# Kernel tuning notes

Measured on AMD Instinct MI355X. Metric: run time of the kernel, lower is better.

## Reference

```python
import jax, jax.numpy as jnp
import numpy as np
import math

IN_CH, KEY_SIZE, VALUE_SIZE = 512, 64, 64
N, T = 4, 4096

def setup_inputs() -> dict:
    key = jax.random.key(0)
    ks = jax.random.split(key, 7)
    s_in = 1.0 / math.sqrt(IN_CH)
    return {
        "x": jax.random.normal(ks[0], (N, T, IN_CH), dtype=jnp.float32),
        "Wq": jax.random.uniform(ks[1], (IN_CH, KEY_SIZE), jnp.float32, -s_in, s_in),
        "bq": jax.random.uniform(ks[2], (KEY_SIZE,), jnp.float32, -s_in, s_in),
        "Wk": jax.random.uniform(ks[3], (IN_CH, KEY_SIZE), jnp.float32, -s_in, s_in),
        "bk": jax.random.uniform(ks[4], (KEY_SIZE,), jnp.float32, -s_in, s_in),
        "Wv": jax.random.uniform(ks[5], (IN_CH, VALUE_SIZE), jnp.float32, -s_in, s_in),
        "bv": jax.random.uniform(ks[6], (VALUE_SIZE,), jnp.float32, -s_in, s_in),
    }

def reference(x, Wq, bq, Wk, bk, Wv, bv):
    # x: [N, T, C]
    Tlen = x.shape[1]
    q = x @ Wq + bq              # [N, T, K]
    k = x @ Wk + bk              # [N, T, K]
    v = x @ Wv + bv              # [N, T, V]
    logits = jnp.einsum('ntk,nsk->nts', q, k)  # [N, T, T]
    # causal mask: strict upper triangle -> -inf (applied BEFORE scaling, as in the original)
    causal = jnp.tril(jnp.ones((Tlen, Tlen), dtype=bool))
    logits = jnp.where(causal, logits, -jnp.inf)
    scale = 1.0 / math.sqrt(Wq.shape[1])
    attn = jax.nn.softmax(logits * scale, axis=-1)
    read = jnp.einsum('nts,nsv->ntv', attn, v)  # [N, T, V]
    return jnp.concatenate((x, read), axis=2)   # [N, T, C+V]
```

## Files before the change

### kernel.cpp

```cpp
#include <hip/hip_runtime.h>
#include <stdint.h>

typedef __attribute__((ext_vector_type(8))) short bf16x8;
typedef __attribute__((ext_vector_type(4))) float f32x4;
typedef __attribute__((ext_vector_type(4))) unsigned short u16x4;
typedef unsigned short u16;

#define NBATCH 4
#define SEQ    4096
#define CIN    512
#define HD     64
#define OC     576
#define NROW   (NBATCH * SEQ)
#define KVB    262144

__device__ __forceinline__ float b2f(u16 u) {
    union { uint32_t i; float f; } w; w.i = ((uint32_t)u) << 16; return w.f;
}
__device__ __forceinline__ u16 f2b(float f) {
    union { float f; uint32_t i; } w; w.f = f;
    uint32_t r = w.i + 0x7fffu + ((w.i >> 16) & 1u);
    return (u16)(r >> 16);
}
__device__ __forceinline__ uint32_t cvtpk_bf16(float a, float b) {
    uint32_t r;
    asm("v_cvt_pk_bf16_f32 %0, %1, %2" : "=v"(r) : "v"(a), "v"(b));
    return r;
}

__global__ void prep_wt(const float* __restrict__ Wq, const float* __restrict__ Wk,
                        const float* __restrict__ Wv, u16* __restrict__ wt) {
    int row = blockIdx.x;
    int g = row >> 6, j = row & 63;
    const float* W = (g == 0) ? Wq : (g == 1) ? Wk : Wv;
    int nt = row >> 4, m = row & 15;
    for (int k = threadIdx.x; k < CIN; k += blockDim.x) {
        int c = k >> 5, qd = (k >> 3) & 3, jj = k & 7;
        size_t off = ((size_t)(nt * 16 + c) * 64 + qd * 16 + m) * 8 + jj;
        wt[off] = f2b(W[k * HD + j]);
    }
}

__global__ __launch_bounds__(256) void proj(
    const float* __restrict__ x, const u16* __restrict__ wt,
    const float* __restrict__ bq, const float* __restrict__ bk, const float* __restrict__ bv,
    u16* __restrict__ qb, u16* __restrict__ kbuf, u16* __restrict__ vtb,
    float* __restrict__ out)
{
    __shared__ __align__(16) float xs[32 * 512];

    int tid = threadIdx.x;
    int lane = tid & 63, w = tid >> 6;
    int m = lane & 15, quad = lane >> 4;
    int r0b = blockIdx.x * 32;

    {
        int rw = w >> 1;
        int pp = (w & 1) * 64 + lane;
#pragma unroll
        for (int k = 0; k < 16; k++) {
            int r = k * 2 + rw;
            int g = pp ^ (r & 15);
            const float* src = x + (size_t)(r0b + r) * CIN + g * 4;
            float* dst = xs + (size_t)(k * 256 + w * 64 + lane) * 4;
            __builtin_amdgcn_global_load_lds(
                (const __attribute__((address_space(1))) void*)src,
                (__attribute__((address_space(3))) void*)dst, 16, 0, 0);
        }
    }
    __syncthreads();

    int ntb = w * 3;

    f32x4 acc0[3], acc1[3];
#pragma unroll
    for (int i = 0; i < 3; i++) {
        acc0[i] = (f32x4){0.f, 0.f, 0.f, 0.f};
        acc1[i] = (f32x4){0.f, 0.f, 0.f, 0.f};
    }

    const float* xrow0 = xs + (size_t)m * 512;
    const float* xrow1 = xs + (size_t)(16 + m) * 512;

#pragma unroll
    for (int c = 0; c < 16; c++) {
        int L0 = c * 8 + quad * 2;
        f32x4 va0 = *(const f32x4*)(xrow0 + (size_t)((L0 ^ m) * 4));
        f32x4 vb0 = *(const f32x4*)(xrow0 + (size_t)(((L0 + 1) ^ m) * 4));
        f32x4 va1 = *(const f32x4*)(xrow1 + (size_t)((L0 ^ m) * 4));
        f32x4 vb1 = *(const f32x4*)(xrow1 + (size_t)(((L0 + 1) ^ m) * 4));
        bf16x8 a0, a1;
        {
            uint32_t* p0 = (uint32_t*)&a0;
            p0[0] = cvtpk_bf16(va0[0], va0[1]);
            p0[1] = cvtpk_bf16(va0[2], va0[3]);
            p0[2] = cvtpk_bf16(vb0[0], vb0[1]);
            p0[3] = cvtpk_bf16(vb0[2], vb0[3]);
            uint32_t* p1 = (uint32_t*)&a1;
            p1[0] = cvtpk_bf16(va1[0], va1[1]);
            p1[1] = cvtpk_bf16(va1[2], va1[3]);
            p1[2] = cvtpk_bf16(vb1[0], vb1[1]);
            p1[3] = cvtpk_bf16(vb1[2], vb1[3]);
        }
#pragma unroll
        for (int t = 0; t < 3; t++) {
            int nt = ntb + t;
            bf16x8 b = *(const bf16x8*)(wt + ((size_t)(nt * 16 + c) * 64 + quad * 16 + m) * 8);
            acc0[t] = __builtin_amdgcn_mfma_f32_16x16x32_bf16(a0, b, acc0[t], 0, 0, 0);
            acc1[t] = __builtin_amdgcn_mfma_f32_16x16x32_bf16(a1, b, acc1[t], 0, 0, 0);
        }
    }

#pragma unroll
    for (int k = 0; k < 16; k++) {
        int G = k * 256 + tid;
        int r = G >> 7, p = G & 127;
        f32x4 v = *(const f32x4*)(xs + (size_t)G * 4);
        int col = (p ^ (r & 15)) * 4;
        *(f32x4*)(out + (size_t)(r0b + r) * OC + col) = v;
    }

    const float SCQ = 0.125f * 1.44269504088896f;

#pragma unroll
    for (int tt = 0; tt < 2; tt++) {
        int r0 = r0b + tt * 16;
        int n  = r0 >> 12;
        int tl = r0 & (SEQ - 1);
#pragma unroll
        for (int t = 0; t < 3; t++) {
            f32x4 acc = tt ? acc1[t] : acc0[t];
            int nt = ntb + t;
            int bi = (nt & 3) * 16 + m;
            if (nt < 4) {
                float biasq = bq[bi];
#pragma unroll
                for (int reg = 0; reg < 4; reg++) {
                    size_t r = (size_t)(r0 + quad * 4 + reg);
                    qb[r * HD + bi] = f2b((acc[reg] + biasq) * SCQ);
                }
            } else if (nt < 8) {
                float biask = bk[bi];
                u16* kbase = kbuf + (size_t)n * KVB
                           + (((size_t)(tl >> 4) * 8 + (bi >> 3)) * 16) * 8 + (bi & 7);
#pragma unroll
                for (int reg = 0; reg < 4; reg++) {
                    int mkey = quad * 4 + reg;
                    kbase[(size_t)mkey * 8] = f2b(acc[reg] + biask);
                }
            } else {
                float biasv = bv[bi];
                u16x4 pk;
#pragma unroll
                for (int reg = 0; reg < 4; reg++) pk[reg] = f2b(acc[reg] + biasv);
                int key0 = tl + quad * 4;
                size_t off = ((((size_t)(bi >> 4) * 128 + (key0 >> 5)) * 4
                               + ((key0 >> 3) & 3)) * 16 + (bi & 15)) * 8 + (key0 & 7);
                *(u16x4*)(vtb + (size_t)n * KVB + off) = pk;
            }
        }
    }
}

__global__ __launch_bounds__(512, 2) void attn(
    const u16* __restrict__ qb, const u16* __restrict__ kbuf,
    const u16* __restrict__ vtb, float* __restrict__ out)
{
    __shared__ __align__(16) union {
        short p[8][16 * 72];
        float o[8][16][68];
    } lu;
    __shared__ float ldsm[8][16];
    __shared__ float ldsl[8][16];

    int tid = threadIdx.x;
    int lane = tid & 63, w = tid >> 6;
    int m = lane & 15, quad = lane >> 4;

    int idx = blockIdx.x;
    int xcd = idx & 7;
    int batch = xcd >> 1;
    int sub = (idx >> 3) * 2 + (xcd & 1);
    int jj = 127 - sub;
    int t0 = jj * 32;
    int nkb = (jj >> 1) + 1;
    int lastkb = nkb - 1;

    const u16* kpb = kbuf + (size_t)batch * KVB;
    const u16* vpb = vtb + (size_t)batch * KVB;

    bf16x8 ones;
#pragma unroll
    for (int i = 0; i < 8; i++) ones[i] = (short)0x3F80;

    const u16* qpb = qb + (size_t)(batch * SEQ + t0 + m) * HD + quad * 8;
    bf16x8 q0[2], q1[2];
#pragma unroll
    for (int q = 0; q < 2; q++) {
        q0[q] = *(const bf16x8*)(qpb + (size_t)(q * 16) * HD);
        q1[q] = *(const bf16x8*)(qpb + (size_t)(q * 16) * HD + 32);
    }

    float mst[2];
    f32x4 o[2][4], ol[2];
#pragma unroll
    for (int q = 0; q < 2; q++) {
        mst[q] = -1e30f;
        ol[q] = (f32x4){0.f, 0.f, 0.f, 0.f};
#pragma unroll
        for (int nt = 0; nt < 4; nt++) o[q][nt] = (f32x4){0.f, 0.f, 0.f, 0.f};
    }

    int cnt = (nkb > w) ? ((nkb - w + 7) >> 3) : 0;
    int kb = w;
    short* pw = &lu.p[w][0];

    bf16x8 k0[4], k1[4];
#pragma unroll
    for (int st = 0; st < 4; st++) {
        k0[st] = *(const bf16x8*)(kpb + (size_t)((kb * 4 + st) * 8 + quad) * 128 + m * 8);
        k1[st] = *(const bf16x8*)(kpb + (size_t)((kb * 4 + st) * 8 + quad + 4) * 128 + m * 8);
    }

    for (int it = 0; it < cnt; it++, kb += 8) {
        int s0 = kb * 64;
        bool diag = (kb == lastkb);

        bf16x8 vf0[4], vf1[4];
#pragma unroll
        for (int nt = 0; nt < 4; nt++) {
            vf0[nt] = *(const bf16x8*)(vpb + (size_t)((nt * 128 + (s0 >> 5)) * 4 + quad) * 128 + m * 8);
            vf1[nt] = *(const bf16x8*)(vpb + (size_t)((nt * 128 + (s0 >> 5) + 1) * 4 + quad) * 128 + m * 8);
        }

        f32x4 s[2][4];
#pragma unroll
        for (int q = 0; q < 2; q++)
#pragma unroll
            for (int st = 0; st < 4; st++) {
                f32x4 a = (f32x4){0.f, 0.f, 0.f, 0.f};
                a = __builtin_amdgcn_mfma_f32_16x16x32_bf16(k0[st], q0[q], a, 0, 0, 0);
                a = __builtin_amdgcn_mfma_f32_16x16x32_bf16(k1[st], q1[q], a, 0, 0, 0);
                s[q][st] = a;
            }

        if (it + 1 < cnt) {
            int kn = kb + 8;
#pragma unroll
            for (int st = 0; st < 4; st++) {
                k0[st] = *(const bf16x8*)(kpb + (size_t)((kn * 4 + st) * 8 + quad) * 128 + m * 8);
                k1[st] = *(const bf16x8*)(kpb + (size_t)((kn * 4 + st) * 8 + quad + 4) * 128 + m * 8);
            }
        }

        if (diag) {
#pragma unroll
            for (int q = 0; q < 2; q++)
#pragma unroll
                for (int st = 0; st < 4; st++)
#pragma unroll
                    for (int r = 0; r < 4; r++) {
                        int key = s0 + st * 16 + quad * 4 + r;
                        if (key > t0 + q * 16 + m) s[q][st][r] = -1e30f;
                    }
        }

        bf16x8 pf0[2], pf1[2];
#pragma unroll
        for (int q = 0; q < 2; q++) {
            float mx = -1e30f;
#pragma unroll
            for (int st = 0; st < 4; st++) {
                float a01 = fmaxf(s[q][st][0], s[q][st][1]);
                float a23 = fmaxf(s[q][st][2], s[q][st][3]);
                mx = fmaxf(mx, fmaxf(a01, a23));
            }
            mx = fmaxf(mx, __shfl_xor(mx, 16, 64));
            mx = fmaxf(mx, __shfl_xor(mx, 32, 64));

            if (__any(mx > mst[q] + 8.0f)) {
                float mn = fmaxf(mst[q], mx);
                float al = exp2f(mst[q] - mn);
#pragma unroll
                for (int nt = 0; nt < 4; nt++)
#pragma unroll
                    for (int r = 0; r < 4; r++) o[q][nt][r] *= al;
                ol[q][0] *= al;
                mst[q] = mn;
            }

#pragma unroll
            for (int st = 0; st < 4; st++) {
                float e0 = exp2f(s[q][st][0] - mst[q]);
                float e1 = exp2f(s[q][st][1] - mst[q]);
                float e2 = exp2f(s[q][st][2] - mst[q]);
                float e3 = exp2f(s[q][st][3] - mst[q]);
                uint2 pk2;
                pk2.x = cvtpk_bf16(e0, e1);
                pk2.y = cvtpk_bf16(e2, e3);
                *(uint2*)(pw + m * 72 + st * 16 + quad * 4) = pk2;
            }
            __asm__ volatile("" ::: "memory");
            pf0[q] = *(const bf16x8*)(pw + m * 72 + quad * 8);
            pf1[q] = *(const bf16x8*)(pw + m * 72 + 32 + quad * 8);
            __asm__ volatile("" ::: "memory");
        }

#pragma unroll
        for (int q = 0; q < 2; q++) {
#pragma unroll
            for (int nt = 0; nt < 4; nt++) {
                o[q][nt] = __builtin_amdgcn_mfma_f32_16x16x32_bf16(vf0[nt], pf0[q], o[q][nt], 0, 0, 0);
                o[q][nt] = __builtin_amdgcn_mfma_f32_16x16x32_bf16(vf1[nt], pf1[q], o[q][nt], 0, 0, 0);
            }
            ol[q] = __builtin_amdgcn_mfma_f32_16x16x32_bf16(ones, pf0[q], ol[q], 0, 0, 0);
            ol[q] = __builtin_amdgcn_mfma_f32_16x16x32_bf16(ones, pf1[q], ol[q], 0, 0, 0);
        }
    }

    __syncthreads();

#pragma unroll
    for (int q = 0; q < 2; q++) {
        if (quad == 0) { ldsm[w][m] = mst[q]; ldsl[w][m] = ol[q][0]; }
#pragma unroll
        for (int nt = 0; nt < 4; nt++)
            *(f32x4*)&lu.o[w][m][nt * 16 + quad * 4] = o[q][nt];
        __syncthreads();

        if (tid < 256) {
            int t = tid >> 4, vg = tid & 15;
            float mmax = -1e30f;
#pragma unroll
            for (int u = 0; u < 8; u++) mmax = fmaxf(mmax, ldsm[u][t]);
            float L = 0.f;
            f32x4 acc = (f32x4){0.f, 0.f, 0.f, 0.f};
#pragma unroll
            for (int u = 0; u < 8; u++) {
                float c = exp2f(ldsm[u][t] - mmax);
                L += ldsl[u][t] * c;
                f32x4 ov = *(const f32x4*)&lu.o[u][t][vg * 4];
#pragma unroll
                for (int i2 = 0; i2 < 4; i2++) acc[i2] += ov[i2] * c;
            }
            float inv = 1.0f / L;
            f32x4 res;
#pragma unroll
            for (int i2 = 0; i2 < 4; i2++) res[i2] = acc[i2] * inv;
            *(f32x4*)(out + (size_t)(batch * SEQ + t0 + q * 16 + t) * OC + CIN + vg * 4) = res;
        }
        __syncthreads();
    }
}

extern "C" void kernel_launch(void* const* d_in, const int* in_sizes, int n_in,
                              void* d_out, int out_size, void* d_ws, size_t ws_size,
                              hipStream_t stream) {
    const float* x  = (const float*)d_in[0];
    const float* Wq = (const float*)d_in[1];
    const float* bq = (const float*)d_in[2];
    const float* Wk = (const float*)d_in[3];
    const float* bk = (const float*)d_in[4];
    const float* Wv = (const float*)d_in[5];
    const float* bv = (const float*)d_in[6];
    float* out = (float*)d_out;

    u16* ws  = (u16*)d_ws;
    u16* wt  = ws;
    u16* qb  = ws + 131072;
    u16* kb  = qb + 16384 * 64;
    u16* vtb = kb + 16384 * 64;

    prep_wt<<<dim3(192), dim3(256), 0, stream>>>(Wq, Wk, Wv, wt);
    proj<<<dim3(512), dim3(256), 0, stream>>>(x, wt, bq, bk, bv, qb, kb, vtb, out);
    attn<<<dim3(512), dim3(512), 0, stream>>>(qb, kb, vtb, out);
}
```

Baseline: 129.1 us.

## Stage Q/K projection outputs in LDS for coalesced stores; raise MFMA wave priority

The projection kernel now writes the Q and K tiles into shared memory (reusing the x staging buffer), then emits them to global memory as 16-byte vectorized stores instead of scattered 2-byte stores. This targets uncoalesced global write traffic in the projection epilogue, at the cost of two extra block barriers and an LDS round trip. Separately, the attention kernel wraps its QK and PV MFMA blocks with s_setprio so waves issuing matrix ops get scheduling priority over waves doing softmax and loads.

```diff
diff --git a/kernel.cpp b/kernel.cpp
--- a/kernel.cpp
+++ b/kernel.cpp
@@ -119,13 +119,17 @@
         int col = (p ^ (r & 15)) * 4;
         *(f32x4*)(out + (size_t)(r0b + r) * OC + col) = v;
     }
-
+    __syncthreads();
+
+    int n0 = r0b >> 12;
     const float SCQ = 0.125f * 1.44269504088896f;
+
+    u16* qt = (u16*)xs;
+    u16* kt = qt + 2048;
 
 #pragma unroll
     for (int tt = 0; tt < 2; tt++) {
         int r0 = r0b + tt * 16;
-        int n  = r0 >> 12;
         int tl = r0 & (SEQ - 1);
 #pragma unroll
         for (int t = 0; t < 3; t++) {
@@ -135,19 +139,13 @@
             if (nt < 4) {
                 float biasq = bq[bi];
 #pragma unroll
-                for (int reg = 0; reg < 4; reg++) {
-                    size_t r = (size_t)(r0 + quad * 4 + reg);
-                    qb[r * HD + bi] = f2b((acc[reg] + biasq) * SCQ);
-                }
+                for (int reg = 0; reg < 4; reg++)
+                    qt[(tt * 16 + quad * 4 + reg) * 64 + bi] = f2b((acc[reg] + biasq) * SCQ);
             } else if (nt < 8) {
                 float biask = bk[bi];
-                u16* kbase = kbuf + (size_t)n * KVB
-                           + (((size_t)(tl >> 4) * 8 + (bi >> 3)) * 16) * 8 + (bi & 7);
-#pragma unroll
-                for (int reg = 0; reg < 4; reg++) {
-                    int mkey = quad * 4 + reg;
-                    kbase[(size_t)mkey * 8] = f2b(acc[reg] + biask);
-                }
+#pragma unroll
+                for (int reg = 0; reg < 4; reg++)
+                    kt[(tt * 16 + quad * 4 + reg) * 64 + bi] = f2b(acc[reg] + biask);
             } else {
                 float biasv = bv[bi];
                 u16x4 pk;
@@ -156,9 +154,24 @@
                 int key0 = tl + quad * 4;
                 size_t off = ((((size_t)(bi >> 4) * 128 + (key0 >> 5)) * 4
                                + ((key0 >> 3) & 3)) * 16 + (bi & 15)) * 8 + (key0 & 7);
-                *(u16x4*)(vtb + (size_t)n * KVB + off) = pk;
-            }
-        }
+                *(u16x4*)(vtb + (size_t)n0 * KVB + off) = pk;
+            }
+        }
+    }
+    __syncthreads();
+
+    {
+        int row = tid >> 3, c8 = (tid & 7) * 8;
+        *(uint4*)(qb + (size_t)(r0b + row) * HD + c8) =
+            *(const uint4*)(qt + row * 64 + c8);
+    }
+    {
+        int tt2 = tid >> 7;
+        int g = (tid & 127) * 8;
+        int key = (g >> 3) & 15, hi = g >> 7;
+        uint4 v = *(const uint4*)(kt + (tt2 * 16 + key) * 64 + hi * 8);
+        size_t gb = (size_t)n0 * KVB + ((size_t)((r0b & (SEQ - 1)) >> 4) + tt2) * 1024 + g;
+        *(uint4*)(kbuf + gb) = v;
     }
 }
 
@@ -234,6 +247,7 @@
         }
 
         f32x4 s[2][4];
+        __builtin_amdgcn_s_setprio(1);
 #pragma unroll
         for (int q = 0; q < 2; q++)
 #pragma unroll
@@ -243,6 +257,7 @@
                 a = __builtin_amdgcn_mfma_f32_16x16x32_bf16(k1[st], q1[q], a, 0, 0, 0);
                 s[q][st] = a;
             }
+        __builtin_amdgcn_s_setprio(0);
 
         if (it + 1 < cnt) {
             int kn = kb + 8;
@@ -306,6 +321,7 @@
             __asm__ volatile("" ::: "memory");
         }
 
+        __builtin_amdgcn_s_setprio(1);
 #pragma unroll
         for (int q = 0; q < 2; q++) {
 #pragma unroll
@@ -316,6 +332,7 @@
             ol[q] = __builtin_amdgcn_mfma_f32_16x16x32_bf16(ones, pf0[q], ol[q], 0, 0, 0);
             ol[q] = __builtin_amdgcn_mfma_f32_16x16x32_bf16(ones, pf1[q], ol[q], 0, 0, 0);
         }
+        __builtin_amdgcn_s_setprio(0);
     }
 
     __syncthreads();
```

Result: no change. 127.5 us (-1.2%).
